# Optimization experiments

Measured on AMD Instinct MI355X. Metric: run time of the kernel, lower is better.

Reference implementation:

```python
import math
import jax, jax.numpy as jnp
import numpy as np

C = 1024  # n_embd
B, T = 4, 2048
H = 4 * C  # mlp hidden
EPS = 1e-5


def setup_inputs() -> dict:
    key = jax.random.key(0)
    ks = jax.random.split(key, 8)
    s = 0.02
    return {
        "x": jax.random.normal(ks[0], (B, T, C), jnp.float32),
        "ln1_g": jnp.ones((C,), jnp.float32),
        "ln1_b": jnp.zeros((C,), jnp.float32),
        "w_attn": jax.random.normal(ks[1], (C, 3 * C), jnp.float32) * s,
        "b_attn": jnp.zeros((3 * C,), jnp.float32),
        "w_proj": jax.random.normal(ks[2], (C, C), jnp.float32) * s,
        "b_proj": jnp.zeros((C,), jnp.float32),
        "ln2_g": jnp.ones((C,), jnp.float32),
        "ln2_b": jnp.zeros((C,), jnp.float32),
        "w_fc": jax.random.normal(ks[3], (C, H), jnp.float32) * s,
        "b_fc": jnp.zeros((H,), jnp.float32),
        "w_mlp_proj": jax.random.normal(ks[4], (H, C), jnp.float32) * s,
        "b_mlp_proj": jnp.zeros((C,), jnp.float32),
    }


def _layernorm(x, g, b):
    mu = jnp.mean(x, axis=-1, keepdims=True)
    var = jnp.mean(jnp.square(x - mu), axis=-1, keepdims=True)
    return (x - mu) * jax.lax.rsqrt(var + EPS) * g + b


def _new_gelu(x):
    c = math.sqrt(2.0 / math.pi)
    return 0.5 * x * (1.0 + jnp.tanh(c * (x + 0.044715 * x * x * x)))


def reference(x, ln1_g, ln1_b, w_attn, b_attn, w_proj, b_proj,
              ln2_g, ln2_b, w_fc, b_fc, w_mlp_proj, b_mlp_proj):
    # --- attention sublayer (single-head, full-dim, no causal mask) ---
    h = _layernorm(x, ln1_g, ln1_b)
    qkv = h @ w_attn + b_attn              # [B,T,3C]
    q, k, v = jnp.split(qkv, 3, axis=-1)   # each [B,T,C]
    scale = 1.0 / math.sqrt(C)
    att = jnp.einsum("btc,bsc->bts", q, k) * scale  # [B,T,T]
    att = jax.nn.softmax(att, axis=-1)
    y = jnp.einsum("bts,bsc->btc", att, v)
    y = y @ w_proj + b_proj
    x = x + y
    # --- MLP sublayer ---
    h2 = _layernorm(x, ln2_g, ln2_b)
    m = _new_gelu(h2 @ w_fc + b_fc) @ w_mlp_proj + b_mlp_proj
    return x + m
```

## Files before the change

### kernel.cpp

```cpp
#include <hip/hip_runtime.h>

typedef __bf16 bf16;
typedef bf16 bf16x8 __attribute__((ext_vector_type(8)));
typedef bf16 bf16x4 __attribute__((ext_vector_type(4)));
typedef float f32x4 __attribute__((ext_vector_type(4)));

#define C_DIM 1024
#define T_DIM 2048
#define B_DIM 4
#define H_DIM 4096

__device__ inline void gld_lds16(const bf16* g, bf16* l) {
    __builtin_amdgcn_global_load_lds(
        (const __attribute__((address_space(1))) unsigned int*)g,
        (__attribute__((address_space(3))) unsigned int*)l,
        16, 0, 0);
}

__device__ inline float fast_gelu(float u) {
    float k2 = 1.5957691216057308f * u + 0.07135480895843475f * u * u * u;
    float t = __expf(-k2);
    return u * __builtin_amdgcn_rcpf(1.0f + t);
}

template <int EPI, typename OutT>
__launch_bounds__(256, 2)
__global__ void gemm8p(const bf16* __restrict__ A, int lda, long long sA,
                       const bf16* __restrict__ Bt, int ldb, long long sB,
                       OutT* __restrict__ Cout, int ldc, long long sC,
                       const float* __restrict__ bias,
                       const float* __restrict__ resid, long long sR,
                       float alpha, int K) {
    const int z = blockIdx.z;
    A += (long long)z * sA;
    Bt += (long long)z * sB;
    Cout += (long long)z * sC;
    if (resid) resid += (long long)z * sR;

    const int rowBase = blockIdx.x * 128;
    const int colBase = blockIdx.y * 128;

    __shared__ __align__(16) bf16 As[2 * 2 * 128 * 32];
    __shared__ __align__(16) bf16 Bs[2 * 2 * 128 * 32];

    const int tid = threadIdx.x;
    const int w = tid >> 6;
    const int lane = tid & 63;
    const int wm = w >> 1, wn = w & 1;
    const int lr = lane & 15, lc = lane >> 4;

    const int gchunk = (tid & 3) ^ ((tid >> 3) & 3);
    const bf16* Ag = A + (size_t)(rowBase + (tid >> 2)) * lda + gchunk * 8;
    const bf16* Bg = Bt + (size_t)(colBase + (tid >> 2)) * ldb + gchunk * 8;
    const size_t ldaL = (size_t)lda, ldbL = (size_t)ldb;
    bf16* AsW = As + w * 512;
    bf16* BsW = Bs + w * 512;

    const int rchunk = lc ^ ((lr >> 1) & 3);
    const int aBase = wm * 2048 + lr * 32 + rchunk * 8;
    const int bBase = wn * 2048 + lr * 32 + rchunk * 8;

#define STAGE(buf, ks, tau) do {                                           \
        const bf16* _ga = Ag + (size_t)(tau) * 64 + (ks) * 32;             \
        bf16* _la = AsW + ((buf) * 2 + (ks)) * 4096;                       \
        gld_lds16(_ga, _la);                                               \
        gld_lds16(_ga + 64 * ldaL, _la + 2048);                            \
        const bf16* _gb = Bg + (size_t)(tau) * 64 + (ks) * 32;             \
        bf16* _lb = BsW + ((buf) * 2 + (ks)) * 4096;                       \
        gld_lds16(_gb, _lb);                                               \
        gld_lds16(_gb + 64 * ldbL, _lb + 2048);                            \
    } while (0)

#define LOAD_AB(buf, ks) do {                                              \
        _Pragma("unroll")                                                  \
        for (int i = 0; i < 4; i++)                                        \
            af[i] = *(const bf16x8*)(As + aBase + ((buf) * 2 + (ks)) * 4096 \
                                     + i * 512);                           \
        _Pragma("unroll")                                                  \
        for (int j = 0; j < 4; j++)                                        \
            bfv[j] = *(const bf16x8*)(Bs + bBase + ((buf) * 2 + (ks)) * 4096 \
                                      + j * 512);                          \
    } while (0)

#define MMAALL() do {                                                      \
        __builtin_amdgcn_s_setprio(1);                                     \
        _Pragma("unroll")                                                  \
        for (int i = 0; i < 4; i++)                                        \
            _Pragma("unroll")                                              \
            for (int j = 0; j < 4; j++)                                    \
                acc[i][j] = __builtin_amdgcn_mfma_f32_16x16x32_bf16(       \
                    af[i], bfv[j], acc[i][j], 0, 0, 0);                    \
        __builtin_amdgcn_s_setprio(0);                                     \
    } while (0)

#define BAR() __builtin_amdgcn_s_barrier()
#define VMC(n) asm volatile("s_waitcnt vmcnt(" #n ")" ::: "memory")

    f32x4 acc[4][4] = {};
    bf16x8 af[4], bfv[4];

    const int NT = K >> 6;

    STAGE(0, 0, 0);
    STAGE(0, 1, 0);
    STAGE(1, 0, 1);
    BAR();

    for (int t = 0; t < NT - 2; t += 2) {
        VMC(8);
        LOAD_AB(0, 0);
        STAGE(1, 1, t + 1);
        BAR(); MMAALL(); BAR();

        VMC(8);
        LOAD_AB(0, 1);
        STAGE(0, 0, t + 2);
        BAR(); MMAALL(); BAR();

        VMC(8);
        LOAD_AB(1, 0);
        STAGE(0, 1, t + 2);
        BAR(); MMAALL(); BAR();

        VMC(8);
        LOAD_AB(1, 1);
        STAGE(1, 0, t + 3);
        BAR(); MMAALL(); BAR();
    }

    VMC(8);
    LOAD_AB(0, 0);
    STAGE(1, 1, NT - 1);
    BAR(); MMAALL(); BAR();

    VMC(8);
    LOAD_AB(0, 1);
    BAR(); MMAALL(); BAR();

    VMC(4);
    LOAD_AB(1, 0);
    BAR(); MMAALL(); BAR();

    VMC(0);
    LOAD_AB(1, 1);
    MMAALL();

#undef STAGE
#undef LOAD_AB
#undef MMAALL
#undef BAR
#undef VMC

    float bval[4];
#pragma unroll
    for (int j = 0; j < 4; j++)
        bval[j] = bias ? bias[colBase + wn * 64 + j * 16 + lr] : 0.0f;

#pragma unroll
    for (int fi = 0; fi < 4; fi++) {
        const int row = rowBase + wm * 64 + fi * 16 + lc * 4;
#pragma unroll
        for (int fj = 0; fj < 4; fj++) {
            const int col = colBase + wn * 64 + fj * 16 + lr;
#pragma unroll
            for (int r = 0; r < 4; r++) {
                float v = acc[fi][fj][r] * alpha + bval[fj];
                if constexpr (EPI == 1) v = fast_gelu(v);
                if constexpr (EPI == 2) v += resid[(size_t)(row + r) * ldc + col];
                Cout[(size_t)(row + r) * ldc + col] = (OutT)v;
            }
        }
    }
}

__launch_bounds__(256)
__global__ void ln_kernel(const float* __restrict__ x, const float* __restrict__ g,
                          const float* __restrict__ b, bf16* __restrict__ out) {
    __shared__ float red[4];
    const int row = blockIdx.x;
    const int tid = threadIdx.x;
    const float4* xr = (const float4*)(x + (size_t)row * C_DIM);
    float4 v = xr[tid];
    float s = v.x + v.y + v.z + v.w;
#pragma unroll
    for (int m = 32; m; m >>= 1) s += __shfl_xor(s, m, 64);
    if ((tid & 63) == 0) red[tid >> 6] = s;
    __syncthreads();
    const float mu = (red[0] + red[1] + red[2] + red[3]) * (1.0f / C_DIM);
    const float dx = v.x - mu, dy = v.y - mu, dz = v.z - mu, dw = v.w - mu;
    float q = dx * dx + dy * dy + dz * dz + dw * dw;
#pragma unroll
    for (int m = 32; m; m >>= 1) q += __shfl_xor(q, m, 64);
    __syncthreads();
    if ((tid & 63) == 0) red[tid >> 6] = q;
    __syncthreads();
    const float var = (red[0] + red[1] + red[2] + red[3]) * (1.0f / C_DIM);
    const float rs = rsqrtf(var + 1e-5f);
    const float4 gg = ((const float4*)g)[tid];
    const float4 bb = ((const float4*)b)[tid];
    bf16x4 o;
    o[0] = (bf16)(dx * rs * gg.x + bb.x);
    o[1] = (bf16)(dy * rs * gg.y + bb.y);
    o[2] = (bf16)(dz * rs * gg.z + bb.z);
    o[3] = (bf16)(dw * rs * gg.w + bb.w);
    ((bf16x4*)(out + (size_t)row * C_DIM))[tid] = o;
}

__launch_bounds__(256)
__global__ void softmax_kernel(const bf16* __restrict__ S, bf16* __restrict__ P) {
    __shared__ float red[4];
    const size_t base = (size_t)blockIdx.x * T_DIM;
    const int tid = threadIdx.x;
    bf16x8 sv = ((const bf16x8*)(S + base))[tid];
    float e[8];
#pragma unroll
    for (int i = 0; i < 8; i++) e[i] = (float)sv[i];
    float mx = e[0];
#pragma unroll
    for (int i = 1; i < 8; i++) mx = fmaxf(mx, e[i]);
#pragma unroll
    for (int m = 32; m; m >>= 1) mx = fmaxf(mx, __shfl_xor(mx, m, 64));
    if ((tid & 63) == 0) red[tid >> 6] = mx;
    __syncthreads();
    mx = fmaxf(fmaxf(red[0], red[1]), fmaxf(red[2], red[3]));
    float s = 0.0f;
#pragma unroll
    for (int i = 0; i < 8; i++) {
        e[i] = __expf(e[i] - mx);
        s += e[i];
    }
#pragma unroll
    for (int m = 32; m; m >>= 1) s += __shfl_xor(s, m, 64);
    __syncthreads();
    if ((tid & 63) == 0) red[tid >> 6] = s;
    __syncthreads();
    const float inv = 1.0f / (red[0] + red[1] + red[2] + red[3]);
    bf16x8 p;
#pragma unroll
    for (int i = 0; i < 8; i++) p[i] = (bf16)(e[i] * inv);
    ((bf16x8*)(P + base))[tid] = p;
}

__global__ void transpose_f2b_all(const float* __restrict__ s0, bf16* __restrict__ d0,
                                  const float* __restrict__ s1, bf16* __restrict__ d1,
                                  const float* __restrict__ s2, bf16* __restrict__ d2,
                                  const float* __restrict__ s3, bf16* __restrict__ d3) {
    __shared__ float tile[32][33];
    int id = blockIdx.x;
    const float* src;
    bf16* dst;
    int R, Cc, local;
    if (id < 3072)       { src = s0; dst = d0; R = 1024; Cc = 3072; local = id; }
    else if (id < 4096)  { src = s1; dst = d1; R = 1024; Cc = 1024; local = id - 3072; }
    else if (id < 8192)  { src = s2; dst = d2; R = 1024; Cc = 4096; local = id - 4096; }
    else                 { src = s3; dst = d3; R = 4096; Cc = 1024; local = id - 8192; }
    const int tilesX = Cc >> 5;
    const int bx = (local % tilesX) * 32;
    const int by = (local / tilesX) * 32;
    const int tx = threadIdx.x, ty = threadIdx.y;
    for (int i = ty; i < 32; i += 8)
        tile[i][tx] = src[(size_t)(by + i) * Cc + bx + tx];
    __syncthreads();
    for (int i = ty; i < 32; i += 8)
        dst[(size_t)(bx + i) * R + by + tx] = (bf16)tile[tx][i];
}

__global__ void transpose_b2b(const bf16* __restrict__ src, int ldsrc, long long sstride,
                              bf16* __restrict__ dst, long long dstride, int R) {
    __shared__ bf16 tile[32][33];
    src += (long long)blockIdx.z * sstride;
    dst += (long long)blockIdx.z * dstride;
    const int bx = blockIdx.x * 32;
    const int by = blockIdx.y * 32;
    const int tx = threadIdx.x, ty = threadIdx.y;
    for (int i = ty; i < 32; i += 8)
        tile[i][tx] = src[(size_t)(by + i) * ldsrc + bx + tx];
    __syncthreads();
    for (int i = ty; i < 32; i += 8)
        dst[(size_t)(bx + i) * R + by + tx] = tile[tx][i];
}

extern "C" void kernel_launch(void* const* d_in, const int* in_sizes, int n_in,
                              void* d_out, int out_size, void* d_ws, size_t ws_size,
                              hipStream_t stream) {
    const float* x      = (const float*)d_in[0];
    const float* ln1_g  = (const float*)d_in[1];
    const float* ln1_b  = (const float*)d_in[2];
    const float* w_attn = (const float*)d_in[3];
    const float* b_attn = (const float*)d_in[4];
    const float* w_proj = (const float*)d_in[5];
    const float* b_proj = (const float*)d_in[6];
    const float* ln2_g  = (const float*)d_in[7];
    const float* ln2_b  = (const float*)d_in[8];
    const float* w_fc   = (const float*)d_in[9];
    const float* b_fc   = (const float*)d_in[10];
    const float* w_mlp  = (const float*)d_in[11];
    const float* b_mlp  = (const float*)d_in[12];
    float* out = (float*)d_out;

    const int M = B_DIM * T_DIM;

    char* base = (char*)d_ws;
    size_t off = 0;
    auto alloc = [&](size_t bytes) -> char* {
        char* p = base + off;
        off += (bytes + 255) & ~(size_t)255;
        return p;
    };
    bf16* wT_attn = (bf16*)alloc((size_t)3072 * 1024 * 2);
    bf16* wT_proj = (bf16*)alloc((size_t)1024 * 1024 * 2);
    bf16* wT_fc   = (bf16*)alloc((size_t)4096 * 1024 * 2);
    bf16* wT_mlp  = (bf16*)alloc((size_t)1024 * 4096 * 2);
    bf16* h       = (bf16*)alloc((size_t)M * 1024 * 2);
    bf16* qkv     = (bf16*)alloc((size_t)M * 3072 * 2);
    bf16* vT      = (bf16*)alloc((size_t)B_DIM * 1024 * 2048 * 2);
    bf16* S       = (bf16*)alloc((size_t)B_DIM * 2048 * 2048 * 2);
    bf16* P       = (bf16*)alloc((size_t)B_DIM * 2048 * 2048 * 2);
    bf16* y       = (bf16*)alloc((size_t)M * 1024 * 2);
    float* x2     = (float*)alloc((size_t)M * 1024 * 4);
    bf16* act     = (bf16*)S;

    const dim3 tb(32, 8);

    transpose_f2b_all<<<12288, tb, 0, stream>>>(w_attn, wT_attn, w_proj, wT_proj,
                                                w_fc, wT_fc, w_mlp, wT_mlp);

    ln_kernel<<<M, 256, 0, stream>>>(x, ln1_g, ln1_b, h);

    gemm8p<0, bf16><<<dim3(64, 24, 1), 256, 0, stream>>>(
        h, 1024, 0, wT_attn, 1024, 0, qkv, 3072, 0, b_attn, nullptr, 0, 1.0f, 1024);

    transpose_b2b<<<dim3(1024 / 32, 2048 / 32, B_DIM), tb, 0, stream>>>(
        qkv + 2 * C_DIM, 3072, (long long)T_DIM * 3072, vT, (long long)C_DIM * T_DIM, T_DIM);

    gemm8p<0, bf16><<<dim3(16, 16, B_DIM), 256, 0, stream>>>(
        qkv, 3072, (long long)T_DIM * 3072,
        qkv + C_DIM, 3072, (long long)T_DIM * 3072,
        S, 2048, (long long)T_DIM * T_DIM, nullptr, nullptr, 0, 0.03125f, 1024);

    softmax_kernel<<<B_DIM * T_DIM, 256, 0, stream>>>(S, P);

    gemm8p<0, bf16><<<dim3(16, 8, B_DIM), 256, 0, stream>>>(
        P, 2048, (long long)T_DIM * T_DIM,
        vT, 2048, (long long)C_DIM * T_DIM,
        y, 1024, (long long)T_DIM * C_DIM, nullptr, nullptr, 0, 1.0f, 2048);

    gemm8p<2, float><<<dim3(64, 8, 1), 256, 0, stream>>>(
        y, 1024, 0, wT_proj, 1024, 0, x2, 1024, 0, b_proj, x, 0, 1.0f, 1024);

    ln_kernel<<<M, 256, 0, stream>>>(x2, ln2_g, ln2_b, h);

    gemm8p<1, bf16><<<dim3(64, 32, 1), 256, 0, stream>>>(
        h, 1024, 0, wT_fc, 1024, 0, act, 4096, 0, b_fc, nullptr, 0, 1.0f, 1024);

    gemm8p<2, float><<<dim3(64, 8, 1), 256, 0, stream>>>(
        act, 4096, 0, wT_mlp, 4096, 0, out, 1024, 0, b_mlp, x2, 0, 1.0f, 4096);
}
```

Before: 516.4 us.

## Use 5-slot ring LDS pipeline in GEMM and fuse V transpose into QKV epilogue

Replaces the two-buffer, two-substage K pipeline with a rotating five-slot ring of 32-wide K stages, keeping several global-to-LDS loads in flight with one barrier pair per step. Adds an epilogue mode to the QKV GEMM that writes the V columns directly in transposed layout, removing the separate transpose kernel and its extra read/write of V. The ring raises LDS usage per block, and the transposed stores are 8-byte strided writes that may coalesce less well.

```diff
diff --git a/kernel.cpp b/kernel.cpp
--- a/kernel.cpp
+++ b/kernel.cpp
@@ -35,13 +35,13 @@
     A += (long long)z * sA;
     Bt += (long long)z * sB;
     Cout += (long long)z * sC;
-    if (resid) resid += (long long)z * sR;
+    if (EPI == 2 && resid) resid += (long long)z * sR;
 
     const int rowBase = blockIdx.x * 128;
     const int colBase = blockIdx.y * 128;
 
-    __shared__ __align__(16) bf16 As[2 * 2 * 128 * 32];
-    __shared__ __align__(16) bf16 Bs[2 * 2 * 128 * 32];
+    __shared__ __align__(16) bf16 As[5 * 128 * 32];
+    __shared__ __align__(16) bf16 Bs[5 * 128 * 32];
 
     const int tid = threadIdx.x;
     const int w = tid >> 6;
@@ -60,26 +60,24 @@
     const int aBase = wm * 2048 + lr * 32 + rchunk * 8;
     const int bBase = wn * 2048 + lr * 32 + rchunk * 8;
 
-#define STAGE(buf, ks, tau) do {                                           \
-        const bf16* _ga = Ag + (size_t)(tau) * 64 + (ks) * 32;             \
-        bf16* _la = AsW + ((buf) * 2 + (ks)) * 4096;                       \
+#define STAGE(so, tau) do {                                                \
+        const bf16* _ga = Ag + (size_t)(tau) * 32;                         \
+        bf16* _la = AsW + (so);                                            \
         gld_lds16(_ga, _la);                                               \
         gld_lds16(_ga + 64 * ldaL, _la + 2048);                            \
-        const bf16* _gb = Bg + (size_t)(tau) * 64 + (ks) * 32;             \
-        bf16* _lb = BsW + ((buf) * 2 + (ks)) * 4096;                       \
+        const bf16* _gb = Bg + (size_t)(tau) * 32;                         \
+        bf16* _lb = BsW + (so);                                            \
         gld_lds16(_gb, _lb);                                               \
         gld_lds16(_gb + 64 * ldbL, _lb + 2048);                            \
     } while (0)
 
-#define LOAD_AB(buf, ks) do {                                              \
+#define LOAD_AB(ro) do {                                                   \
         _Pragma("unroll")                                                  \
         for (int i = 0; i < 4; i++)                                        \
-            af[i] = *(const bf16x8*)(As + aBase + ((buf) * 2 + (ks)) * 4096 \
-                                     + i * 512);                           \
+            af[i] = *(const bf16x8*)(As + aBase + (ro) + i * 512);         \
         _Pragma("unroll")                                                  \
         for (int j = 0; j < 4; j++)                                        \
-            bfv[j] = *(const bf16x8*)(Bs + bBase + ((buf) * 2 + (ks)) * 4096 \
-                                      + j * 512);                          \
+            bfv[j] = *(const bf16x8*)(Bs + bBase + (ro) + j * 512);        \
     } while (0)
 
 #define MMAALL() do {                                                      \
@@ -95,66 +93,79 @@
 
 #define BAR() __builtin_amdgcn_s_barrier()
 #define VMC(n) asm volatile("s_waitcnt vmcnt(" #n ")" ::: "memory")
+#define ROT(x) x = (x == 16384) ? 0 : x + 4096
 
     f32x4 acc[4][4] = {};
     bf16x8 af[4], bfv[4];
 
-    const int NT = K >> 6;
-
-    STAGE(0, 0, 0);
-    STAGE(0, 1, 0);
-    STAGE(1, 0, 1);
+    const int NP = K >> 5;
+
+    STAGE(0, 0);
+    STAGE(4096, 1);
+    STAGE(8192, 2);
+    STAGE(12288, 3);
+    VMC(12);
     BAR();
 
-    for (int t = 0; t < NT - 2; t += 2) {
-        VMC(8);
-        LOAD_AB(0, 0);
-        STAGE(1, 1, t + 1);
-        BAR(); MMAALL(); BAR();
-
-        VMC(8);
-        LOAD_AB(0, 1);
-        STAGE(0, 0, t + 2);
-        BAR(); MMAALL(); BAR();
-
-        VMC(8);
-        LOAD_AB(1, 0);
-        STAGE(0, 1, t + 2);
-        BAR(); MMAALL(); BAR();
-
-        VMC(8);
-        LOAD_AB(1, 1);
-        STAGE(1, 0, t + 3);
-        BAR(); MMAALL(); BAR();
+    int roff = 0, soff = 16384;
+
+    for (int p = 0; p < NP - 4; ++p) {
+        LOAD_AB(roff);
+        STAGE(soff, p + 4);
+        BAR();
+        MMAALL();
+        VMC(12);
+        BAR();
+        ROT(roff); ROT(soff);
     }
 
-    VMC(8);
-    LOAD_AB(0, 0);
-    STAGE(1, 1, NT - 1);
-    BAR(); MMAALL(); BAR();
-
-    VMC(8);
-    LOAD_AB(0, 1);
-    BAR(); MMAALL(); BAR();
-
-    VMC(4);
-    LOAD_AB(1, 0);
-    BAR(); MMAALL(); BAR();
-
-    VMC(0);
-    LOAD_AB(1, 1);
-    MMAALL();
+    LOAD_AB(roff);
+    BAR(); MMAALL();
+    VMC(8); BAR(); ROT(roff);
+
+    LOAD_AB(roff);
+    BAR(); MMAALL();
+    VMC(4); BAR(); ROT(roff);
+
+    LOAD_AB(roff);
+    BAR(); MMAALL();
+    VMC(0); BAR(); ROT(roff);
+
+    LOAD_AB(roff);
+    BAR(); MMAALL();
 
 #undef STAGE
 #undef LOAD_AB
 #undef MMAALL
 #undef BAR
 #undef VMC
+#undef ROT
 
     float bval[4];
 #pragma unroll
     for (int j = 0; j < 4; j++)
         bval[j] = bias ? bias[colBase + wn * 64 + j * 16 + lr] : 0.0f;
+
+    if constexpr (EPI == 3) {
+        if (colBase >= 2048) {
+            bf16* vt = (bf16*)resid;
+#pragma unroll
+            for (int fi = 0; fi < 4; fi++) {
+                const int row = rowBase + wm * 64 + fi * 16 + lc * 4;
+                const int b = row >> 11, t0 = row & 2047;
+#pragma unroll
+                for (int fj = 0; fj < 4; fj++) {
+                    const int vcol = colBase - 2048 + wn * 64 + fj * 16 + lr;
+                    bf16x4 pk;
+#pragma unroll
+                    for (int r = 0; r < 4; r++)
+                        pk[r] = (bf16)(acc[fi][fj][r] * alpha + bval[fj]);
+                    *(bf16x4*)(vt + ((size_t)b * 1024 + vcol) * 2048 + t0) = pk;
+                }
+            }
+            return;
+        }
+    }
 
 #pragma unroll
     for (int fi = 0; fi < 4; fi++) {
@@ -265,21 +276,6 @@
         dst[(size_t)(bx + i) * R + by + tx] = (bf16)tile[tx][i];
 }
 
-__global__ void transpose_b2b(const bf16* __restrict__ src, int ldsrc, long long sstride,
-                              bf16* __restrict__ dst, long long dstride, int R) {
-    __shared__ bf16 tile[32][33];
-    src += (long long)blockIdx.z * sstride;
-    dst += (long long)blockIdx.z * dstride;
-    const int bx = blockIdx.x * 32;
-    const int by = blockIdx.y * 32;
-    const int tx = threadIdx.x, ty = threadIdx.y;
-    for (int i = ty; i < 32; i += 8)
-        tile[i][tx] = src[(size_t)(by + i) * ldsrc + bx + tx];
-    __syncthreads();
-    for (int i = ty; i < 32; i += 8)
-        dst[(size_t)(bx + i) * R + by + tx] = tile[tx][i];
-}
-
 extern "C" void kernel_launch(void* const* d_in, const int* in_sizes, int n_in,
                               void* d_out, int out_size, void* d_ws, size_t ws_size,
                               hipStream_t stream) {
@@ -327,11 +323,9 @@
 
     ln_kernel<<<M, 256, 0, stream>>>(x, ln1_g, ln1_b, h);
 
-    gemm8p<0, bf16><<<dim3(64, 24, 1), 256, 0, stream>>>(
-        h, 1024, 0, wT_attn, 1024, 0, qkv, 3072, 0, b_attn, nullptr, 0, 1.0f, 1024);
-
-    transpose_b2b<<<dim3(1024 / 32, 2048 / 32, B_DIM), tb, 0, stream>>>(
-        qkv + 2 * C_DIM, 3072, (long long)T_DIM * 3072, vT, (long long)C_DIM * T_DIM, T_DIM);
+    gemm8p<3, bf16><<<dim3(64, 24, 1), 256, 0, stream>>>(
+        h, 1024, 0, wT_attn, 1024, 0, qkv, 3072, 0, b_attn,
+        (const float*)vT, 0, 1.0f, 1024);
 
     gemm8p<0, bf16><<<dim3(16, 16, B_DIM), 256, 0, stream>>>(
         qkv, 3072, (long long)T_DIM * 3072,
```

Result: no change. 516.3 us (-0.0%).
